# Kernel optimization log

Measured on AMD Instinct MI355X. Metric: run time of the kernel, lower is better.

Reference implementation:

```python
import jax, jax.numpy as jnp
import numpy as np

B, T, C = 4, 2048, 1024
H = 16                      # n_head
D = C // H                  # head dim = 64
FF = 4 * C                  # 4096


def setup_inputs() -> dict:
    key = jax.random.key(0)
    ks = jax.random.split(key, 9)
    s = 0.02
    return {
        "x": jax.random.normal(ks[0], (B, T, C), dtype=jnp.float32),
        # LayerNorm params (elementwise affine, default torch init)
        "ln1_w": jnp.ones((C,), jnp.float32),
        "ln1_b": jnp.zeros((C,), jnp.float32),
        "ln2_w": jnp.ones((C,), jnp.float32),
        "ln2_b": jnp.zeros((C,), jnp.float32),
        # attention weights, torch Linear layout [out, in], bias=False
        "w_attn": jax.random.normal(ks[1], (3 * C, C), jnp.float32) * s,
        "w_proj": jax.random.normal(ks[2], (C, C), jnp.float32) * s,
        # FFN weights
        "w_fc": jax.random.normal(ks[3], (FF, C), jnp.float32) * s,
        "w_fc_proj": jax.random.normal(ks[4], (C, FF), jnp.float32) * s,
    }


def _layernorm(x, w, b, eps=1e-5):
    mu = jnp.mean(x, axis=-1, keepdims=True)
    var = jnp.var(x, axis=-1, keepdims=True)
    return (x - mu) * jax.lax.rsqrt(var + eps) * w + b


def _attn(h, w_attn, w_proj):
    qkv = jnp.einsum('btc,fc->btf', h, w_attn)        # [B,T,3C]
    q, k, v = jnp.split(qkv, 3, axis=-1)
    q = q.reshape(B, T, H, D).transpose(0, 2, 1, 3)   # [B,H,T,D]
    k = k.reshape(B, T, H, D).transpose(0, 2, 1, 3)
    v = v.reshape(B, T, H, D).transpose(0, 2, 1, 3)
    att = jnp.einsum('bhtd,bhsd->bhts', q, k) * (1.0 / np.sqrt(D))
    causal = jnp.tril(jnp.ones((T, T), dtype=bool))
    att = jnp.where(causal, att, -jnp.inf)
    att = jax.nn.softmax(att, axis=-1)
    y = jnp.einsum('bhts,bhsd->bhtd', att, v)         # [B,H,T,D]
    y = y.transpose(0, 2, 1, 3).reshape(B, T, C)
    return jnp.einsum('btc,oc->bto', y, w_proj)


def _ffn(h, w_fc, w_fc_proj):
    u = jax.nn.gelu(jnp.einsum('btc,fc->btf', h, w_fc), approximate=False)
    return jnp.einsum('btf,cf->btc', u, w_fc_proj)


def reference(x, ln1_w, ln1_b, ln2_w, ln2_b, w_attn, w_proj, w_fc, w_fc_proj):
    x = x + _attn(_layernorm(x, ln1_w, ln1_b), w_attn, w_proj)
    x = x + _ffn(_layernorm(x, ln2_w, ln2_b), w_fc, w_fc_proj)
    return x
```

## Files before the change

kernel.cpp:

```cpp
#include <hip/hip_runtime.h>
#include <hip/hip_bf16.h>

using bf16 = __hip_bfloat16;
typedef __attribute__((ext_vector_type(8))) short short8;
typedef __attribute__((ext_vector_type(4))) short sh4;
typedef __attribute__((ext_vector_type(4))) float f32x4;

#define B_ 4
#define T_ 2048
#define C_ 1024
#define H_ 16
#define FF_ 4096
#define M_TOK (B_ * T_)
#define SCALE2 0.1803368801111f

#define BARRIER() asm volatile("s_barrier" ::: "memory")
#define WAITLGKM0() asm volatile("s_waitcnt lgkmcnt(0)" ::: "memory")
#define WAITLGKM8() asm volatile("s_waitcnt lgkmcnt(8)" ::: "memory")
#define WAITVM4() asm volatile("s_waitcnt vmcnt(4)" ::: "memory")
#define WAITVM2() asm volatile("s_waitcnt vmcnt(2)" ::: "memory")
#define WAITVM0() asm volatile("s_waitcnt vmcnt(0)" ::: "memory")

#define SAE (256 * 64)
#define SBE256 (256 * 64)
#define SBE128 (128 * 64)
#define HALF256 (128 * 64)

__device__ __forceinline__ void gload16(const void* g, void* l) {
    __builtin_amdgcn_global_load_lds(
        (const __attribute__((address_space(1))) void*)g,
        (__attribute__((address_space(3))) void*)l, 16, 0, 0);
}

__device__ __forceinline__ float fexp2(float x) {
    float r;
    asm("v_exp_f32 %0, %1" : "=v"(r) : "v"(x));
    return r;
}

__device__ __forceinline__ float bf16bits2f(short s) {
    return __uint_as_float(((unsigned)(unsigned short)s) << 16);
}

__device__ __forceinline__ unsigned bf2(float a, float b) {
    bf16 x = __float2bfloat16(a), y = __float2bfloat16(b);
    unsigned short ux = *(unsigned short*)&x, uy = *(unsigned short*)&y;
    return (unsigned)ux | ((unsigned)uy << 16);
}

__device__ __forceinline__ float fgelu(float x) {
    float y = 0.79788456f * (x + 0.044715f * x * x * x);
    float tv = fexp2(y * 2.885390082f);
    return x * tv * __builtin_amdgcn_rcpf(tv + 1.f);
}

__global__ __launch_bounds__(256) void prep_kernel(
    const float* __restrict__ x, const float* __restrict__ ln1w, const float* __restrict__ ln1b,
    bf16* __restrict__ ln_out,
    const float* __restrict__ w_attn, const float* __restrict__ w_proj,
    const float* __restrict__ w_fc, const float* __restrict__ w_fcp,
    bf16* __restrict__ wattn_h, bf16* __restrict__ wproj_h,
    bf16* __restrict__ wfc_h, bf16* __restrict__ wfcp_h) {
    const int bid = blockIdx.x;
    const int t = threadIdx.x;
    if (bid < M_TOK) {
        float4 v = ((const float4*)(x + (size_t)bid * C_))[t];
        float s = v.x + v.y + v.z + v.w;
        float s2 = v.x * v.x + v.y * v.y + v.z * v.z + v.w * v.w;
#pragma unroll
        for (int off = 32; off > 0; off >>= 1) {
            s += __shfl_down(s, off);
            s2 += __shfl_down(s2, off);
        }
        __shared__ float ss[4], ss2[4];
        int wave = t >> 6, lane = t & 63;
        if (lane == 0) { ss[wave] = s; ss2[wave] = s2; }
        __syncthreads();
        s = ss[0] + ss[1] + ss[2] + ss[3];
        s2 = ss2[0] + ss2[1] + ss2[2] + ss2[3];
        float mu = s * (1.f / C_);
        float var = s2 * (1.f / C_) - mu * mu;
        float rstd = rsqrtf(var + 1e-5f);
        float4 wv = ((const float4*)ln1w)[t];
        float4 bv = ((const float4*)ln1b)[t];
        uint2 o;
        o.x = bf2((v.x - mu) * rstd * wv.x + bv.x, (v.y - mu) * rstd * wv.y + bv.y);
        o.y = bf2((v.z - mu) * rstd * wv.z + bv.z, (v.w - mu) * rstd * wv.w + bv.w);
        ((uint2*)(ln_out + (size_t)bid * C_))[t] = o;
    } else {
        int i = (bid - M_TOK) * 256 + t;
        const float* src;
        bf16* dst;
        int base;
        if (i < 786432) {
            src = w_attn; dst = wattn_h; base = 0;
        } else if (i < 1048576) {
            src = w_proj; dst = wproj_h; base = 786432;
        } else if (i < 2097152) {
            src = w_fc; dst = wfc_h; base = 1048576;
        } else {
            src = w_fcp; dst = wfcp_h; base = 2097152;
        }
        int j = i - base;
        float4 v = ((const float4*)src)[j];
        uint2 o;
        o.x = bf2(v.x, v.y);
        o.y = bf2(v.z, v.w);
        ((uint2*)dst)[j] = o;
    }
}

__global__ __launch_bounds__(256) void ln_kernel_b(const bf16* __restrict__ x,
                                                   const float* __restrict__ w,
                                                   const float* __restrict__ b,
                                                   bf16* __restrict__ out) {
    int row = blockIdx.x;
    int t = threadIdx.x;
    sh4 h = ((const sh4*)(x + (size_t)row * C_))[t];
    float4 v;
    v.x = bf16bits2f(h[0]);
    v.y = bf16bits2f(h[1]);
    v.z = bf16bits2f(h[2]);
    v.w = bf16bits2f(h[3]);
    float s = v.x + v.y + v.z + v.w;
    float s2 = v.x * v.x + v.y * v.y + v.z * v.z + v.w * v.w;
#pragma unroll
    for (int off = 32; off > 0; off >>= 1) {
        s += __shfl_down(s, off);
        s2 += __shfl_down(s2, off);
    }
    __shared__ float ss[4], ss2[4];
    int wave = t >> 6, lane = t & 63;
    if (lane == 0) { ss[wave] = s; ss2[wave] = s2; }
    __syncthreads();
    s = ss[0] + ss[1] + ss[2] + ss[3];
    s2 = ss2[0] + ss2[1] + ss2[2] + ss2[3];
    float mu = s * (1.f / C_);
    float var = s2 * (1.f / C_) - mu * mu;
    float rstd = rsqrtf(var + 1e-5f);
    float4 wv = ((const float4*)w)[t];
    float4 bv = ((const float4*)b)[t];
    uint2 o;
    o.x = bf2((v.x - mu) * rstd * wv.x + bv.x, (v.y - mu) * rstd * wv.y + bv.y);
    o.y = bf2((v.z - mu) * rstd * wv.z + bv.z, (v.w - mu) * rstd * wv.w + bv.w);
    ((uint2*)(out + (size_t)row * C_))[t] = o;
}

#define STG(ldsbase, g, grow0, k0)                                               \
    {                                                                            \
        _Pragma("unroll") for (int s_ = 0; s_ < 2; s_++) {                       \
            int row_ = s_ * 64 + wid * 8 + sr;                                   \
            gload16(g + (size_t)((grow0) + row_) * K + (k0) + ssc,               \
                    (ldsbase) + row_ * 64 + (lane & 7) * 8);                     \
        }                                                                        \
    }

template <int EPI>
__device__ __forceinline__ void gemm256_dev(short* SAp, short* SBp, int bid,
                                            const bf16* __restrict__ Ag,
                                            const bf16* __restrict__ Bg,
                                            void* __restrict__ Cout,
                                            int M, int N, int K) {
    const int nbx = N >> 8;
    const int nwg = nbx * (M >> 8);
    const int cpx = nwg >> 3;
    const int swzb = (bid & 7) * cpx + (bid >> 3);
    const int m0 = (swzb / nbx) * 256;
    const int n0 = (swzb % nbx) * 256;

    const int t = threadIdx.x;
    const int wid = t >> 6, lane = t & 63;
    const int wm = wid >> 2, wn = wid & 3;
    const int lrow = lane & 15, lg = lane >> 4;
    const int swzr = (lane & 7) * 8;
    const int sr = lane >> 3;
    const int ssc = ((lane & 7) ^ sr) * 8;

    f32x4 acc[8][4];
#pragma unroll
    for (int mi = 0; mi < 8; mi++)
#pragma unroll
        for (int ni = 0; ni < 4; ni++) acc[mi][ni] = (f32x4){0.f, 0.f, 0.f, 0.f};
    short8 bfr[4][2];

    const int T = K >> 6;
    const int niter = T >> 1;

#define DSREADS256(q, buf)                                                       \
    if ((q) == 0) {                                                              \
        _Pragma("unroll") for (int ni = 0; ni < 4; ni++)                         \
        _Pragma("unroll") for (int ks = 0; ks < 2; ks++)                         \
            bfr[ni][ks] = *(const short8*)(&SBp[(buf) * SBE256 +                 \
                (wn * 64 + ni * 16 + lrow) * 64 + ((ks * 32 + lg * 8) ^ swzr)]); \
    }                                                                            \
    _Pragma("unroll") for (int mi2 = 0; mi2 < 2; mi2++)                          \
    _Pragma("unroll") for (int ks = 0; ks < 2; ks++)                             \
        af[mi2 * 2 + ks] = *(const short8*)(&SAp[(buf) * SAE +                   \
            (wm * 128 + (2 * (q) + mi2) * 16 + lrow) * 64 + ((ks * 32 + lg * 8) ^ swzr)]);

#define MFMAS256(q)                                                              \
    __builtin_amdgcn_s_setprio(1);                                               \
    _Pragma("unroll") for (int ks = 0; ks < 2; ks++)                             \
    _Pragma("unroll") for (int ni = 0; ni < 4; ni++)                             \
    _Pragma("unroll") for (int mi2 = 0; mi2 < 2; mi2++)                          \
        acc[2 * (q) + mi2][ni] = __builtin_amdgcn_mfma_f32_16x16x32_bf16(        \
            bfr[ni][ks], af[mi2 * 2 + ks], acc[2 * (q) + mi2][ni], 0, 0, 0);     \
    __builtin_amdgcn_s_setprio(0);

    STG(SAp, Ag, m0, 0);
    STG(SAp + HALF256, Ag, m0 + 128, 0);
    STG(SBp, Bg, n0, 0);
    STG(SBp + HALF256, Bg, n0 + 128, 0);
    STG(SBp + SBE256, Bg, n0, 64);
    STG(SBp + SBE256 + HALF256, Bg, n0 + 128, 64);
    WAITVM4();
    BARRIER();

    for (int iter = 0; iter < niter; iter++) {
        const int tt = 2 * iter;
        const int ka = (tt + 1) * 64, kb = (tt + 2) * 64, kc = (tt + 3) * 64;
        const bool s2 = (tt + 2 < T), s3 = (tt + 3 < T);
        const bool last = (iter == niter - 1);
        short8 af[4];

        DSREADS256(0, 0);
        STG(SAp + SAE, Ag, m0, ka);
        WAITLGKM8();
        BARRIER(); WAITLGKM0(); MFMAS256(0); BARRIER();
        DSREADS256(1, 0);
        STG(SAp + SAE + HALF256, Ag, m0 + 128, ka);
        BARRIER(); WAITLGKM0(); MFMAS256(1); BARRIER();
        DSREADS256(2, 0);
        if (s2) STG(SBp, Bg, n0, kb);
        BARRIER(); WAITLGKM0(); MFMAS256(2); BARRIER();
        DSREADS256(3, 0);
        if (s2) STG(SBp + HALF256, Bg, n0 + 128, kb);
        BARRIER(); WAITLGKM0(); MFMAS256(3);
        if (last) { WAITVM0(); } else { WAITVM4(); }
        BARRIER();
        DSREADS256(0, 1);
        if (s2) STG(SAp, Ag, m0, kb);
        WAITLGKM8();
        BARRIER(); WAITLGKM0(); MFMAS256(0); BARRIER();
        DSREADS256(1, 1);
        if (s2) STG(SAp + HALF256, Ag, m0 + 128, kb);
        BARRIER(); WAITLGKM0(); MFMAS256(1); BARRIER();
        DSREADS256(2, 1);
        if (s3) STG(SBp + SBE256, Bg, n0, kc);
        BARRIER(); WAITLGKM0(); MFMAS256(2); BARRIER();
        DSREADS256(3, 1);
        if (s3) STG(SBp + SBE256 + HALF256, Bg, n0 + 128, kc);
        BARRIER(); WAITLGKM0(); MFMAS256(3);
        if (!last) WAITVM4();
        BARRIER();
    }

#pragma unroll
    for (int mi = 0; mi < 8; mi++) {
        const int gm = m0 + wm * 128 + mi * 16 + lrow;
#pragma unroll
        for (int ni = 0; ni < 4; ni++) {
            const int gn = n0 + wn * 64 + ni * 16 + lg * 4;
            size_t gi = (size_t)gm * N + gn;
            f32x4 a = acc[mi][ni];
            if constexpr (EPI == 0) {
                uint2 o; o.x = bf2(a[0], a[1]); o.y = bf2(a[2], a[3]);
                *(uint2*)&(((bf16*)Cout)[gi]) = o;
            } else if constexpr (EPI == 5) {
                float sc = (gn < C_) ? SCALE2 : 1.f;
                uint2 o; o.x = bf2(a[0] * sc, a[1] * sc); o.y = bf2(a[2] * sc, a[3] * sc);
                *(uint2*)&(((bf16*)Cout)[gi]) = o;
            } else {
                uint2 o;
                o.x = bf2(fgelu(a[0]), fgelu(a[1]));
                o.y = bf2(fgelu(a[2]), fgelu(a[3]));
                *(uint2*)&(((bf16*)Cout)[gi]) = o;
            }
        }
    }
}

template <int EPI>
__device__ __forceinline__ void gemm256x128_dev(short* SAp, short* SBp, int bid,
                                                const bf16* __restrict__ Ag,
                                                const bf16* __restrict__ Bg,
                                                void* __restrict__ Cout,
                                                const void* __restrict__ Res,
                                                int M, int N, int K) {
    const int nbx = N >> 7;
    const int nwg = nbx * (M >> 8);
    const int cpx = nwg >> 3;
    const int swzb = (bid & 7) * cpx + (bid >> 3);
    const int m0 = (swzb / nbx) * 256;
    const int n0 = (swzb % nbx) * 128;

    const int t = threadIdx.x;
    const int wid = t >> 6, lane = t & 63;
    const int wm = wid >> 1, wn = wid & 1;
    const int lrow = lane & 15, lg = lane >> 4;
    const int swzr = (lane & 7) * 8;
    const int sr = lane >> 3;
    const int ssc = ((lane & 7) ^ sr) * 8;

    f32x4 acc[4][4];
#pragma unroll
    for (int mi = 0; mi < 4; mi++)
#pragma unroll
        for (int ni = 0; ni < 4; ni++) acc[mi][ni] = (f32x4){0.f, 0.f, 0.f, 0.f};
    short8 bfr[4][2];

    const int T = K >> 6;
    const int niter = T >> 1;

#define DSRX(p, buf)                                                             \
    if ((p) == 0) {                                                              \
        _Pragma("unroll") for (int ni = 0; ni < 4; ni++)                         \
        _Pragma("unroll") for (int ks = 0; ks < 2; ks++)                         \
            bfr[ni][ks] = *(const short8*)(&SBp[(buf) * SBE128 +                 \
                (wn * 64 + ni * 16 + lrow) * 64 + ((ks * 32 + lg * 8) ^ swzr)]); \
    }                                                                            \
    _Pragma("unroll") for (int mi2 = 0; mi2 < 2; mi2++)                          \
    _Pragma("unroll") for (int ks = 0; ks < 2; ks++)                             \
        af[mi2 * 2 + ks] = *(const short8*)(&SAp[(buf) * SAE +                   \
            (wm * 64 + (2 * (p) + mi2) * 16 + lrow) * 64 + ((ks * 32 + lg * 8) ^ swzr)]);

#define MFX(p)                                                                   \
    __builtin_amdgcn_s_setprio(1);                                               \
    _Pragma("unroll") for (int ks = 0; ks < 2; ks++)                             \
    _Pragma("unroll") for (int ni = 0; ni < 4; ni++)                             \
    _Pragma("unroll") for (int mi2 = 0; mi2 < 2; mi2++)                          \
        acc[2 * (p) + mi2][ni] = __builtin_amdgcn_mfma_f32_16x16x32_bf16(        \
            bfr[ni][ks], af[mi2 * 2 + ks], acc[2 * (p) + mi2][ni], 0, 0, 0);     \
    __builtin_amdgcn_s_setprio(0);

    STG(SAp, Ag, m0, 0);
    STG(SAp + HALF256, Ag, m0 + 128, 0);
    STG(SBp, Bg, n0, 0);
    STG(SBp + SBE128, Bg, n0, 64);
    WAITVM2();
    BARRIER();

    for (int iter = 0; iter < niter; iter++) {
        const int tt = 2 * iter;
        const int ka = (tt + 1) * 64, kb = (tt + 2) * 64, kc = (tt + 3) * 64;
        const bool s2 = (tt + 2 < T), s3 = (tt + 3 < T);
        const bool last = (iter == niter - 1);
        short8 af[4];

        DSRX(0, 0);
        STG(SAp + SAE, Ag, m0, ka);
        STG(SAp + SAE + HALF256, Ag, m0 + 128, ka);
        WAITLGKM8();
        BARRIER(); WAITLGKM0(); MFX(0); BARRIER();
        DSRX(1, 0);
        if (s2) STG(SBp, Bg, n0, kb);
        BARRIER(); WAITLGKM0(); MFX(1);
        if (last) { WAITVM0(); } else { WAITVM2(); }
        BARRIER();
        DSRX(0, 1);
        if (s2) {
            STG(SAp, Ag, m0, kb);
            STG(SAp + HALF256, Ag, m0 + 128, kb);
        }
        WAITLGKM8();
        BARRIER(); WAITLGKM0(); MFX(0); BARRIER();
        DSRX(1, 1);
        if (s3) STG(SBp + SBE128, Bg, n0, kc);
        BARRIER(); WAITLGKM0(); MFX(1);
        if (last) { WAITVM0(); } else { WAITVM2(); }
        BARRIER();
    }

#pragma unroll
    for (int mi = 0; mi < 4; mi++) {
        const int gm = m0 + wm * 64 + mi * 16 + lrow;
#pragma unroll
        for (int ni = 0; ni < 4; ni++) {
            const int gn = n0 + wn * 64 + ni * 16 + lg * 4;
            size_t gi = (size_t)gm * N + gn;
            f32x4 a = acc[mi][ni];
            if constexpr (EPI == 0) {
                uint2 o; o.x = bf2(a[0], a[1]); o.y = bf2(a[2], a[3]);
                *(uint2*)&(((bf16*)Cout)[gi]) = o;
            } else if constexpr (EPI == 3) {
                float4 rv = *(const float4*)&(((const float*)Res)[gi]);
                uint2 o; o.x = bf2(rv.x + a[0], rv.y + a[1]); o.y = bf2(rv.z + a[2], rv.w + a[3]);
                *(uint2*)&(((bf16*)Cout)[gi]) = o;
            } else {
                sh4 hv = *(const sh4*)&(((const bf16*)Res)[gi]);
                float4 o;
                o.x = bf16bits2f(hv[0]) + a[0];
                o.y = bf16bits2f(hv[1]) + a[1];
                o.z = bf16bits2f(hv[2]) + a[2];
                o.w = bf16bits2f(hv[3]) + a[3];
                *(float4*)&(((float*)Cout)[gi]) = o;
            }
        }
    }
}

template <int EPI>
__global__ __launch_bounds__(512, 2) void gemm256(const bf16* __restrict__ Ag,
                                                  const bf16* __restrict__ Bg,
                                                  void* __restrict__ Cout,
                                                  int M, int N, int K) {
    __shared__ short LDS[2 * SAE + 2 * SBE256];
    gemm256_dev<EPI>(LDS, LDS + 2 * SAE, blockIdx.x, Ag, Bg, Cout, M, N, K);
}

template <int EPI>
__global__ __launch_bounds__(512, 2) void gemm256x128(const bf16* __restrict__ Ag,
                                                      const bf16* __restrict__ Bg,
                                                      void* __restrict__ Cout,
                                                      const void* __restrict__ Res,
                                                      int M, int N, int K) {
    __shared__ short LDS[2 * SAE + 2 * SBE128];
    gemm256x128_dev<EPI>(LDS, LDS + 2 * SAE, blockIdx.x, Ag, Bg, Cout, Res, M, N, K);
}

__global__ __launch_bounds__(512, 2) void gemm_qkvt(const bf16* __restrict__ ln_buf,
                                                    const bf16* __restrict__ wattn_h,
                                                    bf16* __restrict__ qk_buf,
                                                    bf16* __restrict__ vt_buf) {
    __shared__ short LDS[2 * SAE + 2 * SBE256];
    if (blockIdx.x < 256) {
        gemm256_dev<5>(LDS, LDS + 2 * SAE, blockIdx.x,
                       ln_buf, wattn_h, qk_buf, M_TOK, 2 * C_, C_);
    } else {
        gemm256x128_dev<0>(LDS, LDS + 2 * SAE, blockIdx.x - 256,
                           wattn_h + (size_t)2 * C_ * C_, ln_buf, vt_buf, nullptr,
                           C_, M_TOK, C_);
    }
}

__global__ __launch_bounds__(256, 4) void flash_attn(const bf16* __restrict__ qk,
                                                     const bf16* __restrict__ vt,
                                                     bf16* __restrict__ y) {
    const int bh = blockIdx.x;
    const int pi = blockIdx.y;
    const int b = bh >> 4, h = bh & 15;
    const int t = threadIdx.x;
    const int wave = t >> 6, lane = t & 63;
    const int lrow = lane & 15, lg = lane >> 4, lk = lg * 8;

    __shared__ alignas(16) short Ks[64 * 72];
    __shared__ alignas(16) short Vs[64 * 72];
    __shared__ alignas(16) short Ps[64 * 72];

    const size_t rs = 2 * C_;
    const bf16* Qg = qk + (size_t)b * T_ * rs + h * 64;
    const bf16* Kg = Qg + C_;
    const bf16* Vg = vt + (size_t)(h * 64) * M_TOK + b * T_;

    const int srow = t >> 3;
    const int sc8 = (t & 7) * 8;

    const int ql = pi, qh = 31 - pi;
    const int nkt = qh + 1;
    const int qgH = qh * 64 + wave * 16 + lrow;
    const int qgL = ql * 64 + wave * 16 + lrow;

    short8 qfH[2], qfL[2];
    {
        const bf16* qr = Qg + (size_t)qgH * rs;
        qfH[0] = *(const short8*)(qr + lk);
        qfH[1] = *(const short8*)(qr + 32 + lk);
        qr = Qg + (size_t)qgL * rs;
        qfL[0] = *(const short8*)(qr + lk);
        qfL[1] = *(const short8*)(qr + 32 + lk);
    }

    f32x4 oH[4], oL[4];
    float mH = -1e30f, lH = 0.f, mL = -1e30f, lL = 0.f;
#pragma unroll
    for (int ni = 0; ni < 4; ni++) {
        oH[ni] = (f32x4){0.f, 0.f, 0.f, 0.f};
        oL[ni] = (f32x4){0.f, 0.f, 0.f, 0.f};
    }

    short8 kr[2], vr[2];
#pragma unroll
    for (int p = 0; p < 2; p++) {
        int r = srow + p * 32;
        kr[p] = *(const short8*)(Kg + (size_t)r * rs + sc8);
        vr[p] = *(const short8*)(Vg + (size_t)r * M_TOK + sc8);
    }

    for (int kt = 0; kt < nkt; kt++) {
        const int s0 = kt * 64;
#pragma unroll
        for (int p = 0; p < 2; p++) {
            int r = srow + p * 32;
            *(short8*)(&Ks[r * 72 + sc8]) = kr[p];
            *(short8*)(&Vs[r * 72 + sc8]) = vr[p];
        }
        __syncthreads();
        if (kt + 1 < nkt) {
            const int s0n = (kt + 1) * 64;
#pragma unroll
            for (int p = 0; p < 2; p++) {
                int r = srow + p * 32;
                kr[p] = *(const short8*)(Kg + (size_t)(s0n + r) * rs + sc8);
                vr[p] = *(const short8*)(Vg + (size_t)r * M_TOK + s0n + sc8);
            }
        }

        {
            f32x4 s[4];
#pragma unroll
            for (int ni = 0; ni < 4; ni++) s[ni] = (f32x4){0.f, 0.f, 0.f, 0.f};
            __builtin_amdgcn_s_setprio(1);
#pragma unroll
            for (int ks = 0; ks < 2; ks++)
#pragma unroll
                for (int ni = 0; ni < 4; ni++) {
                    short8 kf = *(const short8*)(&Ks[(ni * 16 + lrow) * 72 + ks * 32 + lk]);
                    s[ni] = __builtin_amdgcn_mfma_f32_16x16x32_bf16(kf, qfH[ks], s[ni], 0, 0, 0);
                }
            __builtin_amdgcn_s_setprio(0);

            if (kt == qh) {
#pragma unroll
                for (int ni = 0; ni < 4; ni++)
#pragma unroll
                    for (int r = 0; r < 4; r++) {
                        int kvg = s0 + ni * 16 + lg * 4 + r;
                        if (kvg > qgH) s[ni][r] = -1e30f;
                    }
            }

            float pm = s[0][0];
#pragma unroll
            for (int ni = 0; ni < 4; ni++)
#pragma unroll
                for (int r = 0; r < 4; r++) pm = fmaxf(pm, s[ni][r]);
            pm = fmaxf(pm, __shfl_xor(pm, 16));
            pm = fmaxf(pm, __shfl_xor(pm, 32));
            if (!__all(pm - mH <= 8.f)) {
                float mn = fmaxf(mH, pm);
                float alpha = fexp2(mH - mn);
                mH = mn;
                lH *= alpha;
#pragma unroll
                for (int ni = 0; ni < 4; ni++)
#pragma unroll
                    for (int r = 0; r < 4; r++) oH[ni][r] *= alpha;
            }
            float rsum = 0.f;
#pragma unroll
            for (int ni = 0; ni < 4; ni++) {
                float p0 = fexp2(s[ni][0] - mH);
                float p1 = fexp2(s[ni][1] - mH);
                float p2 = fexp2(s[ni][2] - mH);
                float p3 = fexp2(s[ni][3] - mH);
                rsum += (p0 + p1) + (p2 + p3);
                uint2 pk; pk.x = bf2(p0, p1); pk.y = bf2(p2, p3);
                *(uint2*)(&Ps[(wave * 16 + lrow) * 72 + ni * 16 + lg * 4]) = pk;
            }
            rsum += __shfl_xor(rsum, 16);
            rsum += __shfl_xor(rsum, 32);
            lH += rsum;

            __builtin_amdgcn_s_setprio(1);
#pragma unroll
            for (int ks2 = 0; ks2 < 2; ks2++) {
                short8 pf = *(const short8*)(&Ps[(wave * 16 + lrow) * 72 + ks2 * 32 + lk]);
#pragma unroll
                for (int ni = 0; ni < 4; ni++) {
                    short8 vf = *(const short8*)(&Vs[(ni * 16 + lrow) * 72 + ks2 * 32 + lk]);
                    oH[ni] = __builtin_amdgcn_mfma_f32_16x16x32_bf16(vf, pf, oH[ni], 0, 0, 0);
                }
            }
            __builtin_amdgcn_s_setprio(0);
        }

        if (kt <= ql) {
            f32x4 s[4];
#pragma unroll
            for (int ni = 0; ni < 4; ni++) s[ni] = (f32x4){0.f, 0.f, 0.f, 0.f};
            __builtin_amdgcn_s_setprio(1);
#pragma unroll
            for (int ks = 0; ks < 2; ks++)
#pragma unroll
                for (int ni = 0; ni < 4; ni++) {
                    short8 kf = *(const short8*)(&Ks[(ni * 16 + lrow) * 72 + ks * 32 + lk]);
                    s[ni] = __builtin_amdgcn_mfma_f32_16x16x32_bf16(kf, qfL[ks], s[ni], 0, 0, 0);
                }
            __builtin_amdgcn_s_setprio(0);

            if (kt == ql) {
#pragma unroll
                for (int ni = 0; ni < 4; ni++)
#pragma unroll
                    for (int r = 0; r < 4; r++) {
                        int kvg = s0 + ni * 16 + lg * 4 + r;
                        if (kvg > qgL) s[ni][r] = -1e30f;
                    }
            }

            float pm = s[0][0];
#pragma unroll
            for (int ni = 0; ni < 4; ni++)
#pragma unroll
                for (int r = 0; r < 4; r++) pm = fmaxf(pm, s[ni][r]);
            pm = fmaxf(pm, __shfl_xor(pm, 16));
            pm = fmaxf(pm, __shfl_xor(pm, 32));
            if (!__all(pm - mL <= 8.f)) {
                float mn = fmaxf(mL, pm);
                float alpha = fexp2(mL - mn);
                mL = mn;
                lL *= alpha;
#pragma unroll
                for (int ni = 0; ni < 4; ni++)
#pragma unroll
                    for (int r = 0; r < 4; r++) oL[ni][r] *= alpha;
            }
            float rsum = 0.f;
#pragma unroll
            for (int ni = 0; ni < 4; ni++) {
                float p0 = fexp2(s[ni][0] - mL);
                float p1 = fexp2(s[ni][1] - mL);
                float p2 = fexp2(s[ni][2] - mL);
                float p3 = fexp2(s[ni][3] - mL);
                rsum += (p0 + p1) + (p2 + p3);
                uint2 pk; pk.x = bf2(p0, p1); pk.y = bf2(p2, p3);
                *(uint2*)(&Ps[(wave * 16 + lrow) * 72 + ni * 16 + lg * 4]) = pk;
            }
            rsum += __shfl_xor(rsum, 16);
            rsum += __shfl_xor(rsum, 32);
            lL += rsum;

            __builtin_amdgcn_s_setprio(1);
#pragma unroll
            for (int ks2 = 0; ks2 < 2; ks2++) {
                short8 pf = *(const short8*)(&Ps[(wave * 16 + lrow) * 72 + ks2 * 32 + lk]);
#pragma unroll
                for (int ni = 0; ni < 4; ni++) {
                    short8 vf = *(const short8*)(&Vs[(ni * 16 + lrow) * 72 + ks2 * 32 + lk]);
                    oL[ni] = __builtin_amdgcn_mfma_f32_16x16x32_bf16(vf, pf, oL[ni], 0, 0, 0);
                }
            }
            __builtin_amdgcn_s_setprio(0);
        }
        __syncthreads();
    }

    float invH = 1.f / lH, invL = 1.f / lL;
#pragma unroll
    for (int ni = 0; ni < 4; ni++) {
        uint2 pk;
        pk.x = bf2(oH[ni][0] * invH, oH[ni][1] * invH);
        pk.y = bf2(oH[ni][2] * invH, oH[ni][3] * invH);
        *(uint2*)(&y[((size_t)(b * T_ + qgH)) * C_ + h * 64 + ni * 16 + lg * 4]) = pk;
        pk.x = bf2(oL[ni][0] * invL, oL[ni][1] * invL);
        pk.y = bf2(oL[ni][2] * invL, oL[ni][3] * invL);
        *(uint2*)(&y[((size_t)(b * T_ + qgL)) * C_ + h * 64 + ni * 16 + lg * 4]) = pk;
    }
}

extern "C" void kernel_launch(void* const* d_in, const int* in_sizes, int n_in,
                              void* d_out, int out_size, void* d_ws, size_t ws_size,
                              hipStream_t stream) {
    const float* x      = (const float*)d_in[0];
    const float* ln1w   = (const float*)d_in[1];
    const float* ln1b   = (const float*)d_in[2];
    const float* ln2w   = (const float*)d_in[3];
    const float* ln2b   = (const float*)d_in[4];
    const float* w_attn = (const float*)d_in[5];
    const float* w_proj = (const float*)d_in[6];
    const float* w_fc   = (const float*)d_in[7];
    const float* w_fcp  = (const float*)d_in[8];
    float* out = (float*)d_out;

    char* ws = (char*)d_ws;
    bf16* ln_buf  = (bf16*)(ws);
    bf16* qk_buf  = (bf16*)(ws + (16u << 20));
    bf16* vt_buf  = (bf16*)(ws + (48u << 20));
    bf16* ybuf    = (bf16*)(ws + (64u << 20));
    bf16* ubuf    = (bf16*)(ws + (16u << 20));
    bf16* x2b     = (bf16*)(ws + (80u << 20));
    bf16* wattn_h = (bf16*)(ws + (112u << 20));
    bf16* wproj_h = (bf16*)(ws + (118u << 20));
    bf16* wfc_h   = (bf16*)(ws + (120u << 20));
    bf16* wfcp_h  = (bf16*)(ws + (128u << 20));

    prep_kernel<<<M_TOK + 12288, 256, 0, stream>>>(
        x, ln1w, ln1b, ln_buf,
        w_attn, w_proj, w_fc, w_fcp,
        wattn_h, wproj_h, wfc_h, wfcp_h);

    gemm_qkvt<<<512, 512, 0, stream>>>(ln_buf, wattn_h, qk_buf, vt_buf);

    flash_attn<<<dim3(B_ * H_, 16), 256, 0, stream>>>(qk_buf, vt_buf, ybuf);

    gemm256x128<3><<<dim3((M_TOK / 256) * (C_ / 128)), 512, 0, stream>>>(
        ybuf, wproj_h, x2b, x, M_TOK, C_, C_);

    ln_kernel_b<<<M_TOK, 256, 0, stream>>>(x2b, ln2w, ln2b, ln_buf);

    gemm256<2><<<dim3((M_TOK / 256) * (FF_ / 256)), 512, 0, stream>>>(
        ln_buf, wfc_h, ubuf, M_TOK, FF_, C_);

    gemm256x128<4><<<dim3((M_TOK / 256) * (C_ / 128)), 512, 0, stream>>>(
        ubuf, wfcp_h, out, x2b, M_TOK, C_, FF_);
}
```

Baseline: 333.4 us.

## Move remaining weight conversions into flash attention launch to overlap with attention

The fp32-to-bf16 conversion of the proj, fc and fc_proj weights moves out of the prep kernel and into extra blocks appended to the flash attention launch. The launch grid becomes one-dimensional, with the attention tile indices decoded from the block id. The aim is to hide this memory-bound conversion under the compute-bound causal attention and shorten the prep kernel on the critical path before the QKV GEMM. The risk is that the conversion blocks contend with attention blocks for CU slots and bandwidth, and that scheduling order changes which attention tiles start first.

```diff
diff --git a/kernel.cpp b/kernel.cpp
--- a/kernel.cpp
+++ b/kernel.cpp
@@ -57,10 +57,7 @@
 __global__ __launch_bounds__(256) void prep_kernel(
     const float* __restrict__ x, const float* __restrict__ ln1w, const float* __restrict__ ln1b,
     bf16* __restrict__ ln_out,
-    const float* __restrict__ w_attn, const float* __restrict__ w_proj,
-    const float* __restrict__ w_fc, const float* __restrict__ w_fcp,
-    bf16* __restrict__ wattn_h, bf16* __restrict__ wproj_h,
-    bf16* __restrict__ wfc_h, bf16* __restrict__ wfcp_h) {
+    const float* __restrict__ w_attn, bf16* __restrict__ wattn_h) {
     const int bid = blockIdx.x;
     const int t = threadIdx.x;
     if (bid < M_TOK) {
@@ -88,25 +85,12 @@
         o.y = bf2((v.z - mu) * rstd * wv.z + bv.z, (v.w - mu) * rstd * wv.w + bv.w);
         ((uint2*)(ln_out + (size_t)bid * C_))[t] = o;
     } else {
-        int i = (bid - M_TOK) * 256 + t;
-        const float* src;
-        bf16* dst;
-        int base;
-        if (i < 786432) {
-            src = w_attn; dst = wattn_h; base = 0;
-        } else if (i < 1048576) {
-            src = w_proj; dst = wproj_h; base = 786432;
-        } else if (i < 2097152) {
-            src = w_fc; dst = wfc_h; base = 1048576;
-        } else {
-            src = w_fcp; dst = wfcp_h; base = 2097152;
-        }
-        int j = i - base;
-        float4 v = ((const float4*)src)[j];
+        int j = (bid - M_TOK) * 256 + t;
+        float4 v = ((const float4*)w_attn)[j];
         uint2 o;
         o.x = bf2(v.x, v.y);
         o.y = bf2(v.z, v.w);
-        ((uint2*)dst)[j] = o;
+        ((uint2*)wattn_h)[j] = o;
     }
 }
 
@@ -433,13 +417,42 @@
     }
 }
 
-__global__ __launch_bounds__(256, 4) void flash_attn(const bf16* __restrict__ qk,
-                                                     const bf16* __restrict__ vt,
-                                                     bf16* __restrict__ y) {
-    const int bh = blockIdx.x;
-    const int pi = blockIdx.y;
+__global__ __launch_bounds__(256, 4) void flash_cvt(const bf16* __restrict__ qk,
+                                                    const bf16* __restrict__ vt,
+                                                    bf16* __restrict__ y,
+                                                    const float* __restrict__ w_proj,
+                                                    const float* __restrict__ w_fc,
+                                                    const float* __restrict__ w_fcp,
+                                                    bf16* __restrict__ wproj_h,
+                                                    bf16* __restrict__ wfc_h,
+                                                    bf16* __restrict__ wfcp_h) {
+    const int bid = blockIdx.x;
+    const int t = threadIdx.x;
+
+    if (bid >= 1024) {
+        int i = (bid - 1024) * 256 + t;
+        const float* src;
+        bf16* dst;
+        int base;
+        if (i < 262144) {
+            src = w_proj; dst = wproj_h; base = 0;
+        } else if (i < 1310720) {
+            src = w_fc; dst = wfc_h; base = 262144;
+        } else {
+            src = w_fcp; dst = wfcp_h; base = 1310720;
+        }
+        int j = i - base;
+        float4 v = ((const float4*)src)[j];
+        uint2 o;
+        o.x = bf2(v.x, v.y);
+        o.y = bf2(v.z, v.w);
+        ((uint2*)dst)[j] = o;
+        return;
+    }
+
+    const int bh = bid & 63;
+    const int pi = bid >> 6;
     const int b = bh >> 4, h = bh & 15;
-    const int t = threadIdx.x;
     const int wave = t >> 6, lane = t & 63;
     const int lrow = lane & 15, lg = lane >> 4, lk = lg * 8;
 
@@ -684,14 +697,13 @@
     bf16* wfc_h   = (bf16*)(ws + (120u << 20));
     bf16* wfcp_h  = (bf16*)(ws + (128u << 20));
 
-    prep_kernel<<<M_TOK + 12288, 256, 0, stream>>>(
-        x, ln1w, ln1b, ln_buf,
-        w_attn, w_proj, w_fc, w_fcp,
-        wattn_h, wproj_h, wfc_h, wfcp_h);
+    prep_kernel<<<M_TOK + 3072, 256, 0, stream>>>(
+        x, ln1w, ln1b, ln_buf, w_attn, wattn_h);
 
     gemm_qkvt<<<512, 512, 0, stream>>>(ln_buf, wattn_h, qk_buf, vt_buf);
 
-    flash_attn<<<dim3(B_ * H_, 16), 256, 0, stream>>>(qk_buf, vt_buf, ybuf);
+    flash_cvt<<<1024 + 9216, 256, 0, stream>>>(
+        qk_buf, vt_buf, ybuf, w_proj, w_fc, w_fcp, wproj_h, wfc_h, wfcp_h);
 
     gemm256x128<3><<<dim3((M_TOK / 256) * (C_ / 128)), 512, 0, stream>>>(
         ybuf, wproj_h, x2b, x, M_TOK, C_, C_);
```

Result: faster. 326.0 us (-2.2%).
